# Performance work log

Hardware: AMD Instinct MI355X
Metric: run time of the kernel (lower is better)

Reference implementation:

```python
import jax, jax.numpy as jnp
import numpy as np

D, H, DH, FF = 768, 12, 64, 3072

def setup_inputs() -> dict:
    key = jax.random.key(0)
    ks = iter(jax.random.split(key, 40))
    B, Li, Lt = 128, 197, 64
    nrm = lambda shape, s=0.02: (jax.random.normal(next(ks), shape, jnp.float32) * s)
    inp = {}
    inp['image_feats'] = jax.random.normal(next(ks), (B, Li, D), jnp.float32)
    inp['image_att_score'] = jax.random.uniform(next(ks), (B, Li), jnp.float32)
    inp['text_feats'] = jax.random.normal(next(ks), (B, Lt, D), jnp.float32)
    inp['text_att_score'] = jax.random.uniform(next(ks), (B, Lt), jnp.float32)
    inp['tokens'] = jax.random.randint(next(ks), (B, Lt), 0, 1000)
    # BatchNorm1d bottlenecks (inference: running stats)
    for p in ('img', 'txt'):
        inp[f'bn_{p}_g'] = jnp.ones((D,), jnp.float32)
        inp[f'bn_{p}_b'] = jnp.zeros((D,), jnp.float32)
        inp[f'bn_{p}_m'] = nrm((D,), 0.1)
        inp[f'bn_{p}_v'] = jax.random.uniform(next(ks), (D,), jnp.float32, 0.5, 1.5)
    # ResidualAttention (1 layer, cross): ln1, ln2, qkv/out proj, mlp 768->3072->768
    inp['ln1_g'] = jnp.ones((D,), jnp.float32); inp['ln1_b'] = jnp.zeros((D,), jnp.float32)
    inp['ln2_g'] = jnp.ones((D,), jnp.float32); inp['ln2_b'] = jnp.zeros((D,), jnp.float32)
    for n in ('Wq', 'Wk', 'Wv', 'Wo'):
        inp[n] = nrm((D, D))
    for n in ('bq', 'bk', 'bv', 'bo'):
        inp[n] = jnp.zeros((D,), jnp.float32)
    inp['W1'] = nrm((D, FF)); inp['b1'] = jnp.zeros((FF,), jnp.float32)
    inp['W2'] = nrm((FF, D)); inp['b2'] = jnp.zeros((D,), jnp.float32)
    inp['img_K'] = 59   # int(197 * 0.3)
    inp['text_K'] = 19  # int(64 * 0.3)
    return inp

def _ln(x, g, b):
    mu = jnp.mean(x, -1, keepdims=True)
    v = jnp.mean((x - mu) ** 2, -1, keepdims=True)
    return (x - mu) * jax.lax.rsqrt(v + 1e-5) * g + b

def _bn(x, g, b, m, v):
    return (x - m) * jax.lax.rsqrt(v + 1e-5) * g + b

def _cross_block(x, y, key_mask, ln1_g, ln1_b, ln2_g, ln2_b,
                 Wq, bq, Wk, bk, Wv, bv, Wo, bo, W1, b1, W2, b2):
    # cross-attn: queries from x, keys/values from y; pre-LN residual block
    B, Lq, _ = x.shape
    Lk = y.shape[1]
    qn = _ln(x, ln1_g, ln1_b)
    kn = _ln(y, ln1_g, ln1_b)
    q = (qn @ Wq + bq).reshape(B, Lq, H, DH)
    k = (kn @ Wk + bk).reshape(B, Lk, H, DH)
    v = (kn @ Wv + bv).reshape(B, Lk, H, DH)
    scores = jnp.einsum('bqhd,bkhd->bhqk', q, k) / np.float32(np.sqrt(DH))
    if key_mask is not None:  # True = padding -> masked out
        scores = jnp.where(key_mask[:, None, None, :], jnp.float32(-1e9), scores)
    a = jax.nn.softmax(scores, axis=-1)
    att = jnp.einsum('bhqk,bkhd->bqhd', a, v).reshape(B, Lq, D) @ Wo + bo
    x = x + att
    h = _ln(x, ln2_g, ln2_b)
    x = x + jax.nn.gelu(h @ W1 + b1, approximate=False) @ W2 + b2
    return x

def _select(feats, score, K):
    # zero CLS score, full descending sort via top_k, gather token subsets
    L = score.shape[1]
    score = score * jnp.concatenate([jnp.zeros_like(score[:, :1]), jnp.ones_like(score[:, 1:])], axis=1)
    _, idx = jax.lax.top_k(score, L)  # [B, L] sorted desc
    cls = feats[:, :1, :]
    sel1 = jnp.take_along_axis(feats, idx[:, :K, None], axis=1)
    sel2 = jnp.take_along_axis(feats, idx[:, K:2 * K, None], axis=1)
    return jnp.concatenate([cls, sel1], 1), jnp.concatenate([cls, sel2], 1)

def reference(image_feats, image_att_score, text_feats, text_att_score, tokens,
              bn_img_g, bn_img_b, bn_img_m, bn_img_v,
              bn_txt_g, bn_txt_b, bn_txt_m, bn_txt_v,
              ln1_g, ln1_b, ln2_g, ln2_b,
              Wq, bq, Wk, bk, Wv, bv, Wo, bo, W1, b1, W2, b2,
              img_K, text_K):
    blk = lambda x, y, m: _cross_block(x, y, m, ln1_g, ln1_b, ln2_g, ln2_b,
                                       Wq, bq, Wk, bk, Wv, bv, Wo, bo, W1, b1, W2, b2)
    img_global = _bn(image_feats[:, 0, :], bn_img_g, bn_img_b, bn_img_m, bn_img_v)
    text_global = _bn(text_feats[:, 0, :], bn_txt_g, bn_txt_b, bn_txt_m, bn_txt_v)
    text_masks = (tokens == 0)  # True where padding
    img_sel1, img_sel2 = _select(image_feats, image_att_score, img_K)
    image_part1 = blk(img_sel1, image_feats, None)
    image_part2 = blk(img_sel2, image_feats, None)
    txt_sel1, txt_sel2 = _select(text_feats, text_att_score, text_K)
    text_part1 = blk(txt_sel1, text_feats, text_masks)
    text_part2 = blk(txt_sel2, text_feats, text_masks)
    return (img_global, text_global, image_part1, image_part2, text_part1, text_part2)
```

## Files before the change

kernel.cpp:

```cpp
#include <hip/hip_runtime.h>

typedef unsigned short u16;
typedef __bf16 bf16x8 __attribute__((ext_vector_type(8)));
typedef float f32x4 __attribute__((ext_vector_type(4)));

__device__ __forceinline__ float b2f(u16 u) { return __builtin_bit_cast(float, (unsigned)u << 16); }
__device__ __forceinline__ u16 f2b(float f) {
  unsigned x = __builtin_bit_cast(unsigned, f);
  x += 0x7fffu + ((x >> 16) & 1u);
  return (u16)(x >> 16);
}

__device__ __forceinline__ void gload16(const u16* g, u16* l) {
  auto gp = (__attribute__((address_space(1))) void*)(void*)const_cast<u16*>(g);
  auto lp = (__attribute__((address_space(3))) void*)(void*)l;
  __builtin_amdgcn_global_load_lds(gp, lp, 16, 0, 0);
}

__device__ __forceinline__ f32x4 mfma16(bf16x8 a, bf16x8 b, f32x4 c) {
  return __builtin_amdgcn_mfma_f32_16x16x32_bf16(a, b, c, 0, 0, 0);
}

__device__ __forceinline__ float gelu_fast(float v) {
  float u = v * (0.7978845608028654f + 0.03567740813636141f * v * v);
  float e = __expf(2.0f * u);
  float th = 1.0f - 2.0f / (e + 1.0f);
  return 0.5f * v * (1.0f + th);
}

__global__ __launch_bounds__(256) void transpose_k(const float* __restrict__ in, u16* __restrict__ out,
                                                   int R, int C) {
  __shared__ float tile[32][33];
  const int bx = blockIdx.x * 32, by = blockIdx.y * 32;
  const int x = threadIdx.x;
  for (int yy = threadIdx.y; yy < 32; yy += 8) tile[yy][x] = in[(size_t)(by + yy) * C + bx + x];
  __syncthreads();
  for (int yy = threadIdx.y; yy < 32; yy += 8) out[(size_t)(bx + yy) * R + by + x] = f2b(tile[x][yy]);
}

__global__ __launch_bounds__(256) void bn_kernel(const float* __restrict__ feats, int Lrow,
                                                 const float* g, const float* b, const float* m, const float* v,
                                                 float* __restrict__ out) {
  const int bb = blockIdx.x;
  const float* row = feats + (size_t)bb * Lrow * 768;
  for (int d = threadIdx.x; d < 768; d += 256) {
    float x = row[d];
    out[bb * 768 + d] = (x - m[d]) * (1.0f / sqrtf(v[d] + 1e-5f)) * g[d] + b[d];
  }
}

__global__ __launch_bounds__(256) void topk_sel(const float* __restrict__ score, int L, int Ksel,
                                                int* __restrict__ sel, int Lq) {
  __shared__ float s[256];
  const int b = blockIdx.x;
  const int stride2 = 128 * Lq;
  for (int i = threadIdx.x; i < L; i += 256) {
    float v = score[b * L + i];
    s[i] = (i == 0) ? 0.0f : v;
  }
  __syncthreads();
  for (int i = threadIdx.x; i < L; i += 256) {
    float si = s[i];
    int rank = 0;
    for (int j = 0; j < L; ++j) {
      float sj = s[j];
      rank += (sj > si) || (sj == si && j < i);
    }
    if (rank < Ksel) sel[b * Lq + rank + 1] = i;
    else if (rank < 2 * Ksel) sel[stride2 + b * Lq + (rank - Ksel) + 1] = i;
  }
  if (threadIdx.x == 0) { sel[b * Lq] = 0; sel[stride2 + b * Lq] = 0; }
}

__global__ __launch_bounds__(256) void ln_rows(const float* __restrict__ x, const float* g, const float* b,
                                               u16* __restrict__ out) {
  const int row = blockIdx.x * 4 + (threadIdx.x >> 6);
  const int l = threadIdx.x & 63;
  const float* xr = x + (size_t)row * 768;
  float v[12]; float s = 0.f;
#pragma unroll
  for (int i = 0; i < 12; ++i) { v[i] = xr[l + i * 64]; s += v[i]; }
  for (int d = 1; d < 64; d <<= 1) s += __shfl_xor(s, d);
  const float mu = s * (1.0f / 768.0f);
  float q = 0.f;
#pragma unroll
  for (int i = 0; i < 12; ++i) { float t = v[i] - mu; q += t * t; }
  for (int d = 1; d < 64; d <<= 1) q += __shfl_xor(q, d);
  const float rs = 1.0f / sqrtf(q * (1.0f / 768.0f) + 1e-5f);
#pragma unroll
  for (int i = 0; i < 12; ++i) {
    int c = l + i * 64;
    out[(size_t)row * 768 + c] = f2b((v[i] - mu) * rs * g[c] + b[c]);
  }
}

__global__ __launch_bounds__(128) void gather_kernel(const int* __restrict__ sel, const u16* __restrict__ kn,
                                                     const float* __restrict__ feats, u16* __restrict__ qn,
                                                     float* __restrict__ xs, int Lq, int Lsrc) {
  const int q = blockIdx.x, by = blockIdx.y;
  const int p = by >> 7, b = by & 127;
  const int row = (p * 128 + b) * Lq + q;
  const int src = sel[row];
  const uint4* sq = (const uint4*)(kn + ((size_t)b * Lsrc + src) * 768);
  uint4* dq = (uint4*)(qn + (size_t)row * 768);
  for (int c = threadIdx.x; c < 96; c += 128) dq[c] = sq[c];
  const float4* sx = (const float4*)(feats + ((size_t)b * Lsrc + src) * 768);
  float4* dx = (float4*)(xs + (size_t)row * 768);
  for (int c = threadIdx.x; c < 192; c += 128) dx[c] = sx[c];
}

enum { EPI_PLAIN = 0, EPI_QSCALE = 1, EPI_GELU = 2, EPI_RES_FADD = 3, EPI_RES_OUT = 4 };

template <int EPI>
__global__ __launch_bounds__(256) void gemm_bt(const u16* __restrict__ A, const u16* __restrict__ Bt,
                                               const float* __restrict__ bias, const float* __restrict__ res,
                                               void* __restrict__ outp, int M, int N, int K) {
  __shared__ alignas(16) u16 As[2][128 * 64];
  __shared__ alignas(16) u16 Bs[2][128 * 64];
  const int tid = threadIdx.x, l = tid & 63, w = tid >> 6;
  const int nwg = gridDim.x * gridDim.y;
  int lin = blockIdx.y * gridDim.x + blockIdx.x;
  const int q8 = nwg >> 3, r8 = nwg & 7;
  const int xcd = lin & 7, pos = lin >> 3;
  const int nl = (xcd < r8) ? (xcd * (q8 + 1) + pos) : (r8 * (q8 + 1) + (xcd - r8) * q8 + pos);
  const int m0 = (nl / gridDim.x) * 128, n0 = (nl % gridDim.x) * 128;
  const int wm = (w & 1) * 64, wn = (w >> 1) * 64;
  f32x4 acc[4][4] = {};

  auto STAGE = [&](int buf, int k0) {
#pragma unroll
    for (int p = 0; p < 4; ++p) {
      const int s = p * 256 + tid;
      const int row = s >> 3, ch = (s & 7) ^ (row & 7);
      gload16(A + (size_t)(m0 + row) * K + k0 + ch * 8, &As[buf][s * 8]);
      gload16(Bt + (size_t)(n0 + row) * K + k0 + ch * 8, &Bs[buf][s * 8]);
    }
  };
  auto COMPUTE = [&](int buf) {
#pragma unroll
    for (int kk = 0; kk < 2; ++kk) {
      bf16x8 af[4], bfr[4];
#pragma unroll
      for (int i = 0; i < 4; ++i) {
        const int arow = wm + i * 16 + (l & 15);
        af[i] = *(const bf16x8*)&As[buf][arow * 64 + ((((kk * 4 + (l >> 4))) ^ (arow & 7)) << 3)];
        const int brow = wn + i * 16 + (l & 15);
        bfr[i] = *(const bf16x8*)&Bs[buf][brow * 64 + ((((kk * 4 + (l >> 4))) ^ (brow & 7)) << 3)];
      }
#pragma unroll
      for (int mi = 0; mi < 4; ++mi)
#pragma unroll
        for (int ni = 0; ni < 4; ++ni) acc[mi][ni] = mfma16(af[mi], bfr[ni], acc[mi][ni]);
    }
  };

  const int NT = K >> 6;
  STAGE(0, 0);
  int cur = 0;
  for (int t = 0; t < NT - 1; ++t) {
    STAGE(cur ^ 1, (t + 1) << 6);
    asm volatile("s_waitcnt vmcnt(8)" ::: "memory");
    __builtin_amdgcn_sched_barrier(0);
    __builtin_amdgcn_s_barrier();
    COMPUTE(cur);
    __builtin_amdgcn_s_barrier();
    cur ^= 1;
  }
  asm volatile("s_waitcnt vmcnt(0)" ::: "memory");
  __builtin_amdgcn_sched_barrier(0);
  __builtin_amdgcn_s_barrier();
  COMPUTE(cur);

  const int r4 = (l >> 4) * 4, c16 = l & 15;
#pragma unroll
  for (int mi = 0; mi < 4; ++mi) {
#pragma unroll
    for (int ni = 0; ni < 4; ++ni) {
      const int gn = n0 + wn + ni * 16 + c16;
      const float bia = bias[gn];
#pragma unroll
      for (int j = 0; j < 4; ++j) {
        const int gm = m0 + wm + mi * 16 + r4 + j;
        const size_t off = (size_t)gm * N + gn;
        float v = acc[mi][ni][j] + bia;
        if constexpr (EPI == EPI_QSCALE) {
          ((u16*)outp)[off] = f2b(v * 0.125f);
        } else if constexpr (EPI == EPI_GELU) {
          ((u16*)outp)[off] = f2b(gelu_fast(v));
        } else if constexpr (EPI == EPI_RES_FADD || EPI == EPI_RES_OUT) {
          ((float*)outp)[off] = v + res[off];
        } else {
          ((u16*)outp)[off] = f2b(v);
        }
      }
    }
  }
}

template <int LQP, int LKP, int LQ, int LK, bool MASK>
__global__ __launch_bounds__(256) void attn2(const u16* __restrict__ Q, const u16* __restrict__ Kb,
                                             const u16* __restrict__ Vb, const int* __restrict__ toks,
                                             u16* __restrict__ O) {
  constexpr int LKS = LKP + 8;
  const int h = blockIdx.x, by = blockIdx.y;
  const int p = by & 1, bb = by >> 1;
  const int tid = threadIdx.x, l = tid & 63, w = tid >> 6;
  const size_t qrow0 = (size_t)(p * 128 + bb) * LQ;
  const u16* Qg = Q + qrow0 * 768 + h * 64;
  const u16* Kg = Kb + (size_t)bb * LK * 768 + h * 64;
  const u16* Vg = Vb + (size_t)bb * LK * 768 + h * 64;

  __shared__ alignas(16) u16 Qs[LQP * 64];
  __shared__ alignas(16) u16 KV[64 * LKS];
  __shared__ alignas(16) u16 Ss[LQP * LKS];
  __shared__ int tokLds[MASK ? LKP : 1];

  for (int s = tid; s < LQP * 8; s += 256) {
    int row = s >> 3, d8 = (s & 7) ^ (row & 7);
    int gr = row < LQ ? row : LQ - 1;
    gload16(Qg + (size_t)gr * 768 + d8 * 8, &Qs[s * 8]);
  }
  for (int s = tid; s < LKP * 8; s += 256) {
    int row = s >> 3, d8 = (s & 7) ^ (row & 7);
    int gr = row < LK ? row : LK - 1;
    gload16(Kg + (size_t)gr * 768 + d8 * 8, &KV[s * 8]);
  }
  if (MASK)
    for (int c = tid; c < LKP; c += 256) tokLds[c] = (c < LK) ? toks[bb * LK + c] : 1;
  __syncthreads();

  for (int nt = w; nt < LKP / 16; nt += 4) {
    const int brow = nt * 16 + (l & 15);
#pragma unroll
    for (int mt = 0; mt < LQP / 16; ++mt) {
      const int arow = mt * 16 + (l & 15);
      f32x4 a_ = {0.f, 0.f, 0.f, 0.f};
#pragma unroll
      for (int kk = 0; kk < 2; ++kk) {
        bf16x8 av = *(const bf16x8*)&Qs[arow * 64 + (((kk * 4 + (l >> 4)) ^ (arow & 7)) << 3)];
        bf16x8 bv = *(const bf16x8*)&KV[brow * 64 + (((kk * 4 + (l >> 4)) ^ (brow & 7)) << 3)];
        a_ = mfma16(av, bv, a_);
      }
      const int r0 = mt * 16 + (l >> 4) * 4, cc = nt * 16 + (l & 15);
#pragma unroll
      for (int j = 0; j < 4; ++j) Ss[(r0 + j) * LKS + cc] = f2b(a_[j]);
    }
  }
  __syncthreads();

  {
    const int kcol = tid & 31, d8 = tid >> 5;
#pragma unroll
    for (int kb = 0; kb < LKP / 32; ++kb) {
      const int k = kb * 32 + kcol;
      alignas(16) u16 tmp[8] = {0, 0, 0, 0, 0, 0, 0, 0};
      if (k < LK) *(uint4*)tmp = *(const uint4*)(Vg + (size_t)k * 768 + d8 * 8);
#pragma unroll
      for (int j = 0; j < 8; ++j) KV[(d8 * 8 + j) * LKS + k] = tmp[j];
    }
  }
  constexpr int NCH = (LKP + 63) / 64;
  for (int r = w; r < LQ; r += 4) {
    float sv[NCH];
    float mx = -INFINITY;
#pragma unroll
    for (int i = 0; i < NCH; ++i) {
      int c = l + (i << 6);
      float s = -INFINITY;
      if (c < LK) {
        s = b2f(Ss[r * LKS + c]);
        if (MASK && tokLds[c] == 0) s = -1e9f;
      }
      sv[i] = s;
      mx = fmaxf(mx, s);
    }
    for (int d = 1; d < 64; d <<= 1) mx = fmaxf(mx, __shfl_xor(mx, d));
    float sum = 0.f;
#pragma unroll
    for (int i = 0; i < NCH; ++i) { float e = __expf(sv[i] - mx); sv[i] = e; sum += e; }
    for (int d = 1; d < 64; d <<= 1) sum += __shfl_xor(sum, d);
    const float inv = 1.0f / sum;
#pragma unroll
    for (int i = 0; i < NCH; ++i) {
      int c = l + (i << 6);
      if (c < LKP) Ss[r * LKS + c] = f2b(sv[i] * inv);
    }
  }
  __syncthreads();

  for (int mt = w; mt < LQP / 16; mt += 4) {
    const int arow = mt * 16 + (l & 15);
#pragma unroll
    for (int nt = 0; nt < 4; ++nt) {
      f32x4 a_ = {0.f, 0.f, 0.f, 0.f};
#pragma unroll
      for (int kk = 0; kk < LKP; kk += 32) {
        bf16x8 av = *(const bf16x8*)&Ss[arow * LKS + kk + (l >> 4) * 8];
        bf16x8 bv = *(const bf16x8*)&KV[(nt * 16 + (l & 15)) * LKS + kk + (l >> 4) * 8];
        a_ = mfma16(av, bv, a_);
      }
      const int r0 = mt * 16 + (l >> 4) * 4, c16 = l & 15;
#pragma unroll
      for (int j = 0; j < 4; ++j) {
        int r = r0 + j;
        if (r < LQ) O[(qrow0 + r) * 768 + h * 64 + nt * 16 + c16] = f2b(a_[j]);
      }
    }
  }
}

extern "C" void kernel_launch(void* const* d_in, const int* in_sizes, int n_in,
                              void* d_out, int out_size, void* d_ws, size_t ws_size,
                              hipStream_t stream) {
  (void)in_sizes; (void)n_in; (void)out_size; (void)ws_size;
  const float* image_feats = (const float*)d_in[0];
  const float* image_att = (const float*)d_in[1];
  const float* text_feats = (const float*)d_in[2];
  const float* text_att = (const float*)d_in[3];
  const int* tokens = (const int*)d_in[4];
  const float* bn_img_g = (const float*)d_in[5];
  const float* bn_img_b = (const float*)d_in[6];
  const float* bn_img_m = (const float*)d_in[7];
  const float* bn_img_v = (const float*)d_in[8];
  const float* bn_txt_g = (const float*)d_in[9];
  const float* bn_txt_b = (const float*)d_in[10];
  const float* bn_txt_m = (const float*)d_in[11];
  const float* bn_txt_v = (const float*)d_in[12];
  const float* ln1_g = (const float*)d_in[13];
  const float* ln1_b = (const float*)d_in[14];
  const float* ln2_g = (const float*)d_in[15];
  const float* ln2_b = (const float*)d_in[16];
  const float* Wq = (const float*)d_in[17];
  const float* Wk = (const float*)d_in[18];
  const float* Wv = (const float*)d_in[19];
  const float* Wo = (const float*)d_in[20];
  const float* bq = (const float*)d_in[21];
  const float* bk = (const float*)d_in[22];
  const float* bv = (const float*)d_in[23];
  const float* bo = (const float*)d_in[24];
  const float* W1 = (const float*)d_in[25];
  const float* b1 = (const float*)d_in[26];
  const float* W2 = (const float*)d_in[27];
  const float* b2 = (const float*)d_in[28];

  float* out = (float*)d_out;
  char* wsp = (char*)d_ws;
  size_t off = 0;
  auto alloc = [&](size_t bytes) -> void* {
    void* p = wsp + off;
    off += (bytes + 255) & ~(size_t)255;
    return p;
  };
  u16* WqT = (u16*)alloc(768 * 768 * 2);
  u16* WkT = (u16*)alloc(768 * 768 * 2);
  u16* WvT = (u16*)alloc(768 * 768 * 2);
  u16* WoT = (u16*)alloc(768 * 768 * 2);
  u16* W1T = (u16*)alloc((size_t)768 * 3072 * 2);
  u16* W2T = (u16*)alloc((size_t)768 * 3072 * 2);
  char* kvbase = (char*)(wsp + off);
  u16* kn_i = (u16*)alloc((size_t)25216 * 768 * 2);
  u16* Kb_i = (u16*)alloc((size_t)25216 * 768 * 2);
  u16* Vb_i = (u16*)alloc((size_t)25216 * 768 * 2);
  u16* kn_t = (u16*)alloc((size_t)8192 * 768 * 2);
  u16* Kb_t = (u16*)alloc((size_t)8192 * 768 * 2);
  u16* Vb_t = (u16*)alloc((size_t)8192 * 768 * 2);
  u16* gb = (u16*)kvbase;
  int* sel_i = (int*)alloc(2 * 128 * 60 * 4);
  int* sel_t = (int*)alloc(2 * 128 * 20 * 4);
  u16* qn = (u16*)alloc((size_t)20480 * 768 * 2);
  float* xs = (float*)alloc((size_t)20480 * 768 * 4);
  u16* Qb = (u16*)alloc((size_t)20480 * 768 * 2);

  const dim3 tb(32, 8);
  transpose_k<<<dim3(24, 24), tb, 0, stream>>>(Wq, WqT, 768, 768);
  transpose_k<<<dim3(24, 24), tb, 0, stream>>>(Wk, WkT, 768, 768);
  transpose_k<<<dim3(24, 24), tb, 0, stream>>>(Wv, WvT, 768, 768);
  transpose_k<<<dim3(24, 24), tb, 0, stream>>>(Wo, WoT, 768, 768);
  transpose_k<<<dim3(96, 24), tb, 0, stream>>>(W1, W1T, 768, 3072);
  transpose_k<<<dim3(24, 96), tb, 0, stream>>>(W2, W2T, 3072, 768);

  bn_kernel<<<128, 256, 0, stream>>>(image_feats, 197, bn_img_g, bn_img_b, bn_img_m, bn_img_v, out);
  bn_kernel<<<128, 256, 0, stream>>>(text_feats, 64, bn_txt_g, bn_txt_b, bn_txt_m, bn_txt_v, out + 98304);

  topk_sel<<<128, 256, 0, stream>>>(image_att, 197, 59, sel_i, 60);
  topk_sel<<<128, 256, 0, stream>>>(text_att, 64, 19, sel_t, 20);

  ln_rows<<<25216 / 4, 256, 0, stream>>>(image_feats, ln1_g, ln1_b, kn_i);
  gemm_bt<EPI_PLAIN><<<dim3(6, 197), 256, 0, stream>>>(kn_i, WkT, bk, nullptr, Kb_i, 25216, 768, 768);
  gemm_bt<EPI_PLAIN><<<dim3(6, 197), 256, 0, stream>>>(kn_i, WvT, bv, nullptr, Vb_i, 25216, 768, 768);
  ln_rows<<<8192 / 4, 256, 0, stream>>>(text_feats, ln1_g, ln1_b, kn_t);
  gemm_bt<EPI_PLAIN><<<dim3(6, 64), 256, 0, stream>>>(kn_t, WkT, bk, nullptr, Kb_t, 8192, 768, 768);
  gemm_bt<EPI_PLAIN><<<dim3(6, 64), 256, 0, stream>>>(kn_t, WvT, bv, nullptr, Vb_t, 8192, 768, 768);

  gather_kernel<<<dim3(60, 256), 128, 0, stream>>>(sel_i, kn_i, image_feats, qn, xs, 60, 197);
  gather_kernel<<<dim3(20, 256), 128, 0, stream>>>(sel_t, kn_t, text_feats, qn + (size_t)15360 * 768,
                                                   xs + (size_t)15360 * 768, 20, 64);

  gemm_bt<EPI_QSCALE><<<dim3(6, 160), 256, 0, stream>>>(qn, WqT, bq, nullptr, Qb, 20480, 768, 768);

  attn2<64, 224, 60, 197, false><<<dim3(12, 256), 256, 0, stream>>>(Qb, Kb_i, Vb_i, nullptr, qn);
  attn2<32, 64, 20, 64, true><<<dim3(12, 256), 256, 0, stream>>>(Qb + (size_t)15360 * 768, Kb_t, Vb_t,
                                                                 tokens, qn + (size_t)15360 * 768);

  gemm_bt<EPI_RES_FADD><<<dim3(6, 160), 256, 0, stream>>>(qn, WoT, bo, xs, xs, 20480, 768, 768);
  ln_rows<<<20480 / 4, 256, 0, stream>>>(xs, ln2_g, ln2_b, Qb);
  gemm_bt<EPI_GELU><<<dim3(24, 160), 256, 0, stream>>>(Qb, W1T, b1, nullptr, gb, 20480, 3072, 768);
  gemm_bt<EPI_RES_OUT><<<dim3(6, 160), 256, 0, stream>>>(gb, W2T, b2, xs, out + 196608, 20480, 768, 3072);
}
```

Baseline: 755.5 us.

## Add 256x256 tile GEMM kernel with 512 threads for large projections

Introduces a gemm256 kernel using 256x256 output tiles, 8 waves and a two-stage prefetch (stage t+2 after compute), and switches the image K/V, Q, O, FFN1 and FFN2 GEMMs to it. It also wraps the MFMA blocks in s_setprio to raise wave priority during math. The larger tiles aim to raise arithmetic intensity and cut global/L2 traffic per FLOP. The costs are 128 KB of LDS per block, which limits occupancy, and fewer workgroups (for example 240 for the 768-wide GEMMs), which risks poor CU utilization. Image K/V buffers are enlarged to 25344 rows so M is padded to the tile size; the GEMM now reads padding rows past the 25216 written by ln_rows, and those rows may hold garbage.

Result: slower. 813.5 us (+7.7%).

```diff
diff --git a/kernel.cpp b/kernel.cpp
--- a/kernel.cpp
+++ b/kernel.cpp
@@ -110,6 +110,21 @@
 }
 
 enum { EPI_PLAIN = 0, EPI_QSCALE = 1, EPI_GELU = 2, EPI_RES_FADD = 3, EPI_RES_OUT = 4 };
+
+__device__ __forceinline__ void epi_store(int EPI_ignored, float v, size_t off, void* outp, const float* res);
+
+template <int EPI>
+__device__ __forceinline__ void epi_write(float v, size_t off, void* outp, const float* res) {
+  if constexpr (EPI == EPI_QSCALE) {
+    ((u16*)outp)[off] = f2b(v * 0.125f);
+  } else if constexpr (EPI == EPI_GELU) {
+    ((u16*)outp)[off] = f2b(gelu_fast(v));
+  } else if constexpr (EPI == EPI_RES_FADD || EPI == EPI_RES_OUT) {
+    ((float*)outp)[off] = v + res[off];
+  } else {
+    ((u16*)outp)[off] = f2b(v);
+  }
+}
 
 template <int EPI>
 __global__ __launch_bounds__(256) void gemm_bt(const u16* __restrict__ A, const u16* __restrict__ Bt,
@@ -147,10 +162,12 @@
         const int brow = wn + i * 16 + (l & 15);
         bfr[i] = *(const bf16x8*)&Bs[buf][brow * 64 + ((((kk * 4 + (l >> 4))) ^ (brow & 7)) << 3)];
       }
+      __builtin_amdgcn_s_setprio(1);
 #pragma unroll
       for (int mi = 0; mi < 4; ++mi)
 #pragma unroll
         for (int ni = 0; ni < 4; ++ni) acc[mi][ni] = mfma16(af[mi], bfr[ni], acc[mi][ni]);
+      __builtin_amdgcn_s_setprio(0);
     }
   };
 
@@ -173,7 +190,7 @@
 
   const int r4 = (l >> 4) * 4, c16 = l & 15;
 #pragma unroll
-  for (int mi = 0; mi < 4; ++mi) {
+  for (int mi = 0; mi < 4; ++mi)
 #pragma unroll
     for (int ni = 0; ni < 4; ++ni) {
       const int gn = n0 + wn + ni * 16 + c16;
@@ -181,20 +198,94 @@
 #pragma unroll
       for (int j = 0; j < 4; ++j) {
         const int gm = m0 + wm + mi * 16 + r4 + j;
-        const size_t off = (size_t)gm * N + gn;
-        float v = acc[mi][ni][j] + bia;
-        if constexpr (EPI == EPI_QSCALE) {
-          ((u16*)outp)[off] = f2b(v * 0.125f);
-        } else if constexpr (EPI == EPI_GELU) {
-          ((u16*)outp)[off] = f2b(gelu_fast(v));
-        } else if constexpr (EPI == EPI_RES_FADD || EPI == EPI_RES_OUT) {
-          ((float*)outp)[off] = v + res[off];
-        } else {
-          ((u16*)outp)[off] = f2b(v);
-        }
-      }
-    }
-  }
+        epi_write<EPI>(acc[mi][ni][j] + bia, (size_t)gm * N + gn, outp, res);
+      }
+    }
+}
+
+template <int EPI>
+__global__ __launch_bounds__(512, 2) void gemm256(const u16* __restrict__ A, const u16* __restrict__ Bt,
+                                                  const float* __restrict__ bias, const float* __restrict__ res,
+                                                  void* __restrict__ outp, int M, int N, int K) {
+  __shared__ alignas(16) u16 As[2][256 * 64];
+  __shared__ alignas(16) u16 Bs[2][256 * 64];
+  const int tid = threadIdx.x, l = tid & 63, w = tid >> 6;
+  const int nwg = gridDim.x * gridDim.y;
+  int lin = blockIdx.y * gridDim.x + blockIdx.x;
+  const int q8 = nwg >> 3, r8 = nwg & 7;
+  const int xcd = lin & 7, pos = lin >> 3;
+  const int nl = (xcd < r8) ? (xcd * (q8 + 1) + pos) : (r8 * (q8 + 1) + (xcd - r8) * q8 + pos);
+  const int m0 = (nl / gridDim.x) * 256, n0 = (nl % gridDim.x) * 256;
+  const int wr = w >> 2, wc = w & 3;
+  f32x4 acc[8][4] = {};
+
+  auto STAGE = [&](int buf, int k0) {
+#pragma unroll
+    for (int i = 0; i < 4; ++i) {
+      const int s = i * 512 + tid;
+      const int row = s >> 3, ch = (s & 7) ^ (row & 7);
+      gload16(A + (size_t)(m0 + row) * K + k0 + ch * 8, &As[buf][s * 8]);
+    }
+#pragma unroll
+    for (int i = 0; i < 4; ++i) {
+      const int s = i * 512 + tid;
+      const int row = s >> 3, ch = (s & 7) ^ (row & 7);
+      gload16(Bt + (size_t)(n0 + row) * K + k0 + ch * 8, &Bs[buf][s * 8]);
+    }
+  };
+
+  auto COMPUTE = [&](int buf) {
+#pragma unroll
+    for (int kk = 0; kk < 2; ++kk) {
+      bf16x8 bfr[4], af[8];
+#pragma unroll
+      for (int j = 0; j < 4; ++j) {
+        const int brow = wc * 64 + j * 16 + (l & 15);
+        bfr[j] = *(const bf16x8*)&Bs[buf][brow * 64 + (((kk * 4 + (l >> 4)) ^ (brow & 7)) << 3)];
+      }
+#pragma unroll
+      for (int i = 0; i < 8; ++i) {
+        const int arow = wr * 128 + i * 16 + (l & 15);
+        af[i] = *(const bf16x8*)&As[buf][arow * 64 + (((kk * 4 + (l >> 4)) ^ (arow & 7)) << 3)];
+      }
+      __builtin_amdgcn_s_setprio(1);
+#pragma unroll
+      for (int i = 0; i < 8; ++i)
+#pragma unroll
+        for (int j = 0; j < 4; ++j) acc[i][j] = mfma16(af[i], bfr[j], acc[i][j]);
+      __builtin_amdgcn_s_setprio(0);
+    }
+  };
+
+  const int NT = K >> 6;
+  STAGE(0, 0);
+  STAGE(1, 64);
+  for (int t = 0; t < NT; ++t) {
+    if (t < NT - 1) {
+      asm volatile("s_waitcnt vmcnt(8)" ::: "memory");
+    } else {
+      asm volatile("s_waitcnt vmcnt(0)" ::: "memory");
+    }
+    __builtin_amdgcn_sched_barrier(0);
+    __builtin_amdgcn_s_barrier();
+    COMPUTE(t & 1);
+    __builtin_amdgcn_s_barrier();
+    if (t + 2 < NT) STAGE(t & 1, (t + 2) << 6);
+  }
+
+  const int r4 = (l >> 4) * 4, c16 = l & 15;
+#pragma unroll
+  for (int i = 0; i < 8; ++i)
+#pragma unroll
+    for (int j = 0; j < 4; ++j) {
+      const int gn = n0 + wc * 64 + j * 16 + c16;
+      const float bia = bias[gn];
+#pragma unroll
+      for (int jj = 0; jj < 4; ++jj) {
+        const int gm = m0 + wr * 128 + i * 16 + r4 + jj;
+        epi_write<EPI>(acc[i][j][jj] + bia, (size_t)gm * N + gn, outp, res);
+      }
+    }
 }
 
 template <int LQP, int LKP, int LQ, int LK, bool MASK>
@@ -358,9 +449,9 @@
   u16* W1T = (u16*)alloc((size_t)768 * 3072 * 2);
   u16* W2T = (u16*)alloc((size_t)768 * 3072 * 2);
   char* kvbase = (char*)(wsp + off);
-  u16* kn_i = (u16*)alloc((size_t)25216 * 768 * 2);
-  u16* Kb_i = (u16*)alloc((size_t)25216 * 768 * 2);
-  u16* Vb_i = (u16*)alloc((size_t)25216 * 768 * 2);
+  u16* kn_i = (u16*)alloc((size_t)25344 * 768 * 2);
+  u16* Kb_i = (u16*)alloc((size_t)25344 * 768 * 2);
+  u16* Vb_i = (u16*)alloc((size_t)25344 * 768 * 2);
   u16* kn_t = (u16*)alloc((size_t)8192 * 768 * 2);
   u16* Kb_t = (u16*)alloc((size_t)8192 * 768 * 2);
   u16* Vb_t = (u16*)alloc((size_t)8192 * 768 * 2);
@@ -386,8 +477,8 @@
   topk_sel<<<128, 256, 0, stream>>>(text_att, 64, 19, sel_t, 20);
 
   ln_rows<<<25216 / 4, 256, 0, stream>>>(image_feats, ln1_g, ln1_b, kn_i);
-  gemm_bt<EPI_PLAIN><<<dim3(6, 197), 256, 0, stream>>>(kn_i, WkT, bk, nullptr, Kb_i, 25216, 768, 768);
-  gemm_bt<EPI_PLAIN><<<dim3(6, 197), 256, 0, stream>>>(kn_i, WvT, bv, nullptr, Vb_i, 25216, 768, 768);
+  gemm256<EPI_PLAIN><<<dim3(3, 99), 512, 0, stream>>>(kn_i, WkT, bk, nullptr, Kb_i, 25344, 768, 768);
+  gemm256<EPI_PLAIN><<<dim3(3, 99), 512, 0, stream>>>(kn_i, WvT, bv, nullptr, Vb_i, 25344, 768, 768);
   ln_rows<<<8192 / 4, 256, 0, stream>>>(text_feats, ln1_g, ln1_b, kn_t);
   gemm_bt<EPI_PLAIN><<<dim3(6, 64), 256, 0, stream>>>(kn_t, WkT, bk, nullptr, Kb_t, 8192, 768, 768);
   gemm_bt<EPI_PLAIN><<<dim3(6, 64), 256, 0, stream>>>(kn_t, WvT, bv, nullptr, Vb_t, 8192, 768, 768);
@@ -396,14 +487,14 @@
   gather_kernel<<<dim3(20, 256), 128, 0, stream>>>(sel_t, kn_t, text_feats, qn + (size_t)15360 * 768,
                                                    xs + (size_t)15360 * 768, 20, 64);
 
-  gemm_bt<EPI_QSCALE><<<dim3(6, 160), 256, 0, stream>>>(qn, WqT, bq, nullptr, Qb, 20480, 768, 768);
+  gemm256<EPI_QSCALE><<<dim3(3, 80), 512, 0, stream>>>(qn, WqT, bq, nullptr, Qb, 20480, 768, 768);
 
   attn2<64, 224, 60, 197, false><<<dim3(12, 256), 256, 0, stream>>>(Qb, Kb_i, Vb_i, nullptr, qn);
   attn2<32, 64, 20, 64, true><<<dim3(12, 256), 256, 0, stream>>>(Qb + (size_t)15360 * 768, Kb_t, Vb_t,
                                                                  tokens, qn + (size_t)15360 * 768);
 
-  gemm_bt<EPI_RES_FADD><<<dim3(6, 160), 256, 0, stream>>>(qn, WoT, bo, xs, xs, 20480, 768, 768);
+  gemm256<EPI_RES_FADD><<<dim3(3, 80), 512, 0, stream>>>(qn, WoT, bo, xs, xs, 20480, 768, 768);
   ln_rows<<<20480 / 4, 256, 0, stream>>>(xs, ln2_g, ln2_b, Qb);
-  gemm_bt<EPI_GELU><<<dim3(24, 160), 256, 0, stream>>>(Qb, W1T, b1, nullptr, gb, 20480, 3072, 768);
-  gemm_bt<EPI_RES_OUT><<<dim3(6, 160), 256, 0, stream>>>(gb, W2T, b2, xs, out + 196608, 20480, 768, 3072);
-}
+  gemm256<EPI_GELU><<<dim3(12, 80), 512, 0, stream>>>(Qb, W1T, b1, nullptr, gb, 20480, 3072, 768);
+  gemm256<EPI_RES_OUT><<<dim3(3, 80), 512, 0, stream>>>(gb, W2T, b2, xs, out + 196608, 20480, 768, 3072);
+}
```

## Fuse K and V projections into one interleaved GEMM and batch weight transposes

Applied to the files above, without the earlier changes.

Concatenates the transposed Wk and Wv into one 1536-wide weight and runs a single GEMM per modality, writing K and V interleaved per row, with attention reading them at a 1536 stride. The four 768x768 weight transposes are merged into one launch, and the K/V bias is concatenated with device-to-device copies. The MFMA inner loop is also wrapped in s_setprio to favour the compute wave. This removes launches and a second read of the LN'd activations, but the interleaved K/V layout makes attention loads strided, and kvbase/gb aliasing now spans a larger region.

Result: no change. 748.1 us (-1.0%).

```diff
diff --git a/kernel.cpp b/kernel.cpp
--- a/kernel.cpp
+++ b/kernel.cpp
@@ -36,6 +36,21 @@
   for (int yy = threadIdx.y; yy < 32; yy += 8) tile[yy][x] = in[(size_t)(by + yy) * C + bx + x];
   __syncthreads();
   for (int yy = threadIdx.y; yy < 32; yy += 8) out[(size_t)(bx + yy) * R + by + x] = f2b(tile[x][yy]);
+}
+
+__global__ __launch_bounds__(256) void transpose4(const float* __restrict__ i0, const float* __restrict__ i1,
+                                                  const float* __restrict__ i2, const float* __restrict__ i3,
+                                                  u16* __restrict__ o0, u16* __restrict__ o1,
+                                                  u16* __restrict__ o2, u16* __restrict__ o3) {
+  __shared__ float tile[32][33];
+  const int z = blockIdx.z;
+  const float* in = (z == 0) ? i0 : (z == 1) ? i1 : (z == 2) ? i2 : i3;
+  u16* out = (z == 0) ? o0 : (z == 1) ? o1 : (z == 2) ? o2 : o3;
+  const int bx = blockIdx.x * 32, by = blockIdx.y * 32;
+  const int x = threadIdx.x;
+  for (int yy = threadIdx.y; yy < 32; yy += 8) tile[yy][x] = in[(size_t)(by + yy) * 768 + bx + x];
+  __syncthreads();
+  for (int yy = threadIdx.y; yy < 32; yy += 8) out[(size_t)(bx + yy) * 768 + by + x] = f2b(tile[x][yy]);
 }
 
 __global__ __launch_bounds__(256) void bn_kernel(const float* __restrict__ feats, int Lrow,
@@ -110,6 +125,19 @@
 }
 
 enum { EPI_PLAIN = 0, EPI_QSCALE = 1, EPI_GELU = 2, EPI_RES_FADD = 3, EPI_RES_OUT = 4 };
+
+template <int EPI>
+__device__ __forceinline__ void epi_write(float v, size_t off, void* outp, const float* res) {
+  if constexpr (EPI == EPI_QSCALE) {
+    ((u16*)outp)[off] = f2b(v * 0.125f);
+  } else if constexpr (EPI == EPI_GELU) {
+    ((u16*)outp)[off] = f2b(gelu_fast(v));
+  } else if constexpr (EPI == EPI_RES_FADD || EPI == EPI_RES_OUT) {
+    ((float*)outp)[off] = v + res[off];
+  } else {
+    ((u16*)outp)[off] = f2b(v);
+  }
+}
 
 template <int EPI>
 __global__ __launch_bounds__(256) void gemm_bt(const u16* __restrict__ A, const u16* __restrict__ Bt,
@@ -147,10 +175,12 @@
         const int brow = wn + i * 16 + (l & 15);
         bfr[i] = *(const bf16x8*)&Bs[buf][brow * 64 + ((((kk * 4 + (l >> 4))) ^ (brow & 7)) << 3)];
       }
+      __builtin_amdgcn_s_setprio(1);
 #pragma unroll
       for (int mi = 0; mi < 4; ++mi)
 #pragma unroll
         for (int ni = 0; ni < 4; ++ni) acc[mi][ni] = mfma16(af[mi], bfr[ni], acc[mi][ni]);
+      __builtin_amdgcn_s_setprio(0);
     }
   };
 
@@ -173,7 +203,7 @@
 
   const int r4 = (l >> 4) * 4, c16 = l & 15;
 #pragma unroll
-  for (int mi = 0; mi < 4; ++mi) {
+  for (int mi = 0; mi < 4; ++mi)
 #pragma unroll
     for (int ni = 0; ni < 4; ++ni) {
       const int gn = n0 + wn + ni * 16 + c16;
@@ -181,34 +211,22 @@
 #pragma unroll
       for (int j = 0; j < 4; ++j) {
         const int gm = m0 + wm + mi * 16 + r4 + j;
-        const size_t off = (size_t)gm * N + gn;
-        float v = acc[mi][ni][j] + bia;
-        if constexpr (EPI == EPI_QSCALE) {
-          ((u16*)outp)[off] = f2b(v * 0.125f);
-        } else if constexpr (EPI == EPI_GELU) {
-          ((u16*)outp)[off] = f2b(gelu_fast(v));
-        } else if constexpr (EPI == EPI_RES_FADD || EPI == EPI_RES_OUT) {
-          ((float*)outp)[off] = v + res[off];
-        } else {
-          ((u16*)outp)[off] = f2b(v);
-        }
-      }
-    }
-  }
+        epi_write<EPI>(acc[mi][ni][j] + bia, (size_t)gm * N + gn, outp, res);
+      }
+    }
 }
 
 template <int LQP, int LKP, int LQ, int LK, bool MASK>
-__global__ __launch_bounds__(256) void attn2(const u16* __restrict__ Q, const u16* __restrict__ Kb,
-                                             const u16* __restrict__ Vb, const int* __restrict__ toks,
-                                             u16* __restrict__ O) {
+__global__ __launch_bounds__(256) void attn2(const u16* __restrict__ Q, const u16* __restrict__ KVb,
+                                             const int* __restrict__ toks, u16* __restrict__ O) {
   constexpr int LKS = LKP + 8;
   const int h = blockIdx.x, by = blockIdx.y;
   const int p = by & 1, bb = by >> 1;
   const int tid = threadIdx.x, l = tid & 63, w = tid >> 6;
   const size_t qrow0 = (size_t)(p * 128 + bb) * LQ;
   const u16* Qg = Q + qrow0 * 768 + h * 64;
-  const u16* Kg = Kb + (size_t)bb * LK * 768 + h * 64;
-  const u16* Vg = Vb + (size_t)bb * LK * 768 + h * 64;
+  const u16* Kg = KVb + (size_t)bb * LK * 1536 + h * 64;
+  const u16* Vg = Kg + 768;
 
   __shared__ alignas(16) u16 Qs[LQP * 64];
   __shared__ alignas(16) u16 KV[64 * LKS];
@@ -223,7 +241,7 @@
   for (int s = tid; s < LKP * 8; s += 256) {
     int row = s >> 3, d8 = (s & 7) ^ (row & 7);
     int gr = row < LK ? row : LK - 1;
-    gload16(Kg + (size_t)gr * 768 + d8 * 8, &KV[s * 8]);
+    gload16(Kg + (size_t)gr * 1536 + d8 * 8, &KV[s * 8]);
   }
   if (MASK)
     for (int c = tid; c < LKP; c += 256) tokLds[c] = (c < LK) ? toks[bb * LK + c] : 1;
@@ -254,7 +272,7 @@
     for (int kb = 0; kb < LKP / 32; ++kb) {
       const int k = kb * 32 + kcol;
       alignas(16) u16 tmp[8] = {0, 0, 0, 0, 0, 0, 0, 0};
-      if (k < LK) *(uint4*)tmp = *(const uint4*)(Vg + (size_t)k * 768 + d8 * 8);
+      if (k < LK) *(uint4*)tmp = *(const uint4*)(Vg + (size_t)k * 1536 + d8 * 8);
 #pragma unroll
       for (int j = 0; j < 8; ++j) KV[(d8 * 8 + j) * LKS + k] = tmp[j];
     }
@@ -352,18 +370,16 @@
     return p;
   };
   u16* WqT = (u16*)alloc(768 * 768 * 2);
-  u16* WkT = (u16*)alloc(768 * 768 * 2);
-  u16* WvT = (u16*)alloc(768 * 768 * 2);
+  u16* WkvT = (u16*)alloc((size_t)1536 * 768 * 2);
   u16* WoT = (u16*)alloc(768 * 768 * 2);
   u16* W1T = (u16*)alloc((size_t)768 * 3072 * 2);
   u16* W2T = (u16*)alloc((size_t)768 * 3072 * 2);
+  float* bkv = (float*)alloc(1536 * 4);
   char* kvbase = (char*)(wsp + off);
   u16* kn_i = (u16*)alloc((size_t)25216 * 768 * 2);
-  u16* Kb_i = (u16*)alloc((size_t)25216 * 768 * 2);
-  u16* Vb_i = (u16*)alloc((size_t)25216 * 768 * 2);
+  u16* KVb_i = (u16*)alloc((size_t)25216 * 1536 * 2);
   u16* kn_t = (u16*)alloc((size_t)8192 * 768 * 2);
-  u16* Kb_t = (u16*)alloc((size_t)8192 * 768 * 2);
-  u16* Vb_t = (u16*)alloc((size_t)8192 * 768 * 2);
+  u16* KVb_t = (u16*)alloc((size_t)8192 * 1536 * 2);
   u16* gb = (u16*)kvbase;
   int* sel_i = (int*)alloc(2 * 128 * 60 * 4);
   int* sel_t = (int*)alloc(2 * 128 * 20 * 4);
@@ -372,12 +388,11 @@
   u16* Qb = (u16*)alloc((size_t)20480 * 768 * 2);
 
   const dim3 tb(32, 8);
-  transpose_k<<<dim3(24, 24), tb, 0, stream>>>(Wq, WqT, 768, 768);
-  transpose_k<<<dim3(24, 24), tb, 0, stream>>>(Wk, WkT, 768, 768);
-  transpose_k<<<dim3(24, 24), tb, 0, stream>>>(Wv, WvT, 768, 768);
-  transpose_k<<<dim3(24, 24), tb, 0, stream>>>(Wo, WoT, 768, 768);
+  transpose4<<<dim3(24, 24, 4), tb, 0, stream>>>(Wq, Wk, Wv, Wo, WqT, WkvT, WkvT + (size_t)768 * 768, WoT);
   transpose_k<<<dim3(96, 24), tb, 0, stream>>>(W1, W1T, 768, 3072);
   transpose_k<<<dim3(24, 96), tb, 0, stream>>>(W2, W2T, 3072, 768);
+  hipMemcpyAsync(bkv, bk, 768 * 4, hipMemcpyDeviceToDevice, stream);
+  hipMemcpyAsync(bkv + 768, bv, 768 * 4, hipMemcpyDeviceToDevice, stream);
 
   bn_kernel<<<128, 256, 0, stream>>>(image_feats, 197, bn_img_g, bn_img_b, bn_img_m, bn_img_v, out);
   bn_kernel<<<128, 256, 0, stream>>>(text_feats, 64, bn_txt_g, bn_txt_b, bn_txt_m, bn_txt_v, out + 98304);
@@ -386,11 +401,9 @@
   topk_sel<<<128, 256, 0, stream>>>(text_att, 64, 19, sel_t, 20);
 
   ln_rows<<<25216 / 4, 256, 0, stream>>>(image_feats, ln1_g, ln1_b, kn_i);
-  gemm_bt<EPI_PLAIN><<<dim3(6, 197), 256, 0, stream>>>(kn_i, WkT, bk, nullptr, Kb_i, 25216, 768, 768);
-  gemm_bt<EPI_PLAIN><<<dim3(6, 197), 256, 0, stream>>>(kn_i, WvT, bv, nullptr, Vb_i, 25216, 768, 768);
+  gemm_bt<EPI_PLAIN><<<dim3(12, 197), 256, 0, stream>>>(kn_i, WkvT, bkv, nullptr, KVb_i, 25216, 1536, 768);
   ln_rows<<<8192 / 4, 256, 0, stream>>>(text_feats, ln1_g, ln1_b, kn_t);
-  gemm_bt<EPI_PLAIN><<<dim3(6, 64), 256, 0, stream>>>(kn_t, WkT, bk, nullptr, Kb_t, 8192, 768, 768);
-  gemm_bt<EPI_PLAIN><<<dim3(6, 64), 256, 0, stream>>>(kn_t, WvT, bv, nullptr, Vb_t, 8192, 768, 768);
+  gemm_bt<EPI_PLAIN><<<dim3(12, 64), 256, 0, stream>>>(kn_t, WkvT, bkv, nullptr, KVb_t, 8192, 1536, 768);
 
   gather_kernel<<<dim3(60, 256), 128, 0, stream>>>(sel_i, kn_i, image_feats, qn, xs, 60, 197);
   gather_kernel<<<dim3(20, 256), 128, 0, stream>>>(sel_t, kn_t, text_feats, qn + (size_t)15360 * 768,
@@ -398,8 +411,8 @@
 
   gemm_bt<EPI_QSCALE><<<dim3(6, 160), 256, 0, stream>>>(qn, WqT, bq, nullptr, Qb, 20480, 768, 768);
 
-  attn2<64, 224, 60, 197, false><<<dim3(12, 256), 256, 0, stream>>>(Qb, Kb_i, Vb_i, nullptr, qn);
-  attn2<32, 64, 20, 64, true><<<dim3(12, 256), 256, 0, stream>>>(Qb + (size_t)15360 * 768, Kb_t, Vb_t,
+  attn2<64, 224, 60, 197, false><<<dim3(12, 256), 256, 0, stream>>>(Qb, KVb_i, nullptr, qn);
+  attn2<32, 64, 20, 64, true><<<dim3(12, 256), 256, 0, stream>>>(Qb + (size_t)15360 * 768, KVb_t,
                                                                  tokens, qn + (size_t)15360 * 768);
 
   gemm_bt<EPI_RES_FADD><<<dim3(6, 160), 256, 0, stream>>>(qn, WoT, bo, xs, xs, 20480, 768, 768);
```
